# Optimization experiments

Measured on AMD Instinct MI355X. Metric: run time of the kernel, lower is better.

Reference implementation:

```python
import jax, jax.numpy as jnp
import numpy as np

D_MODEL = 2048
N_HEADS = 16
D_HEAD = 128
ROPE_THETA = 10000.0


def _rope(x, offset):
    # x: [B, H, S, D]; half-rotation RoPE with position offset
    B, H, S, D = x.shape
    inv_freq = 1.0 / (ROPE_THETA ** (jnp.arange(0, D, 2, dtype=jnp.float32) / D))  # [D/2]
    pos = (offset + jnp.arange(S, dtype=jnp.float32))                              # [S]
    ang = pos[:, None] * inv_freq[None, :]                                         # [S, D/2]
    cos = jnp.cos(ang).astype(x.dtype)
    sin = jnp.sin(ang).astype(x.dtype)
    x1, x2 = x[..., : D // 2], x[..., D // 2 :]
    return jnp.concatenate([x1 * cos - x2 * sin, x2 * cos + x1 * sin], axis=-1)


def setup_inputs() -> dict:
    key = jax.random.key(0)
    ks = jax.random.split(key, 5)
    B, Sq, Skv = 4, 1024, 1024
    x = jax.random.normal(ks[0], (B, Sq, D_MODEL), dtype=jnp.float32)
    cache_k = jax.random.normal(ks[1], (B, N_HEADS, Skv, D_HEAD), dtype=jnp.float32)
    cache_v = jax.random.normal(ks[2], (B, N_HEADS, Skv, D_HEAD), dtype=jnp.float32)
    w_qkv = jax.random.normal(ks[3], (D_MODEL, 3 * D_MODEL), dtype=jnp.float32) * (D_MODEL ** -0.5)
    w_o = jax.random.normal(ks[4], (D_MODEL, D_MODEL), dtype=jnp.float32) * (D_MODEL ** -0.5)
    return {"x": x, "cache_k": cache_k, "cache_v": cache_v, "w_qkv": w_qkv, "w_o": w_o}


def reference(x, cache_k, cache_v, w_qkv, w_o):
    B, S, _ = x.shape
    offset = cache_k.shape[2]
    # fused QKV projection: [B, S, 3*d_model] -> [B, H, S, 3*d_head]
    qkv = jnp.einsum("bsd,de->bse", x, w_qkv)
    qkv = qkv.reshape(B, S, N_HEADS, 3 * D_HEAD).transpose(0, 2, 1, 3)
    q, k, v = jnp.split(qkv, 3, axis=-1)
    q = _rope(q, offset)
    k = _rope(k, offset)
    # KV-cache concat along sequence dim
    k = jnp.concatenate([cache_k, k], axis=2)  # [B, H, Skv+S, D]
    v = jnp.concatenate([cache_v, v], axis=2)
    # SDPA (no mask, matching mask=None path)
    scale = D_HEAD ** -0.5
    scores = jnp.einsum("bhqd,bhkd->bhqk", q, k) * scale
    attn = jax.nn.softmax(scores, axis=-1)
    out = jnp.einsum("bhqk,bhkd->bhqd", attn, v)           # [B, H, S, D]
    out = out.transpose(0, 2, 1, 3).reshape(B, S, D_MODEL)
    return jnp.einsum("bsd,de->bse", out, w_o)
```

## Files before the change

kernel.cpp:

```cpp
#include <hip/hip_runtime.h>


typedef __bf16 bf16x8 __attribute__((ext_vector_type(8)));
typedef float f32x4 __attribute__((ext_vector_type(4)));
typedef unsigned short u16x8 __attribute__((ext_vector_type(8)));
typedef unsigned short u16x4 __attribute__((ext_vector_type(4)));

__device__ __forceinline__ float b2f(unsigned short u) {
  return __builtin_bit_cast(float, (unsigned int)u << 16);
}
__device__ __forceinline__ unsigned short f2b(float f) {
  unsigned int x = __builtin_bit_cast(unsigned int, f);
  x += 0x7fffu + ((x >> 16) & 1u);
  return (unsigned short)(x >> 16);
}
__device__ __forceinline__ unsigned int cvt_pk_bf16(float lo, float hi) {
  unsigned int r;
  asm("v_cvt_pk_bf16_f32 %0, %1, %2" : "=v"(r) : "v"(lo), "v"(hi));
  return r;
}
__device__ __forceinline__ void gload_lds16(const void* g, void* l) {
  __builtin_amdgcn_global_load_lds(
      (__attribute__((address_space(1))) void*)(g),
      (__attribute__((address_space(3))) void*)(l), 16, 0, 0);
}
__device__ __forceinline__ void barrier_nodrain() {
  asm volatile("" ::: "memory");
  __builtin_amdgcn_s_barrier();
  asm volatile("" ::: "memory");
}

__global__ void build_trig(float* __restrict__ cs, float* __restrict__ sn) {
  int idx = blockIdx.x * 256 + threadIdx.x;
  int s = idx >> 6, i = idx & 63;
  float inv = exp2f(-(float)i * (13.287712379549449f / 64.0f));
  float ang = (float)(1024 + s) * inv;
  cs[idx] = cosf(ang);
  sn[idx] = sinf(ang);
}

__global__ void conv_bf16(const float* __restrict__ in, unsigned short* __restrict__ out) {
  size_t i = ((size_t)blockIdx.x * 256 + threadIdx.x) * 8;
  float4 a = *(const float4*)(in + i);
  float4 b = *(const float4*)(in + i + 4);
  u16x8 v;
  v[0] = f2b(a.x); v[1] = f2b(a.y); v[2] = f2b(a.z); v[3] = f2b(a.w);
  v[4] = f2b(b.x); v[5] = f2b(b.y); v[6] = f2b(b.z); v[7] = f2b(b.w);
  *(u16x8*)(out + i) = v;
}

__global__ __launch_bounds__(256) void transpose_conv(
    const float* __restrict__ in, unsigned short* __restrict__ out, int R, int C) {
  __shared__ float tile[32][33];
  int c0 = blockIdx.x * 32, r0 = blockIdx.y * 32;
  int tx = threadIdx.x & 31, ty = threadIdx.x >> 5;
#pragma unroll
  for (int j = 0; j < 4; ++j)
    tile[ty + j * 8][tx] = in[(size_t)(r0 + ty + j * 8) * C + c0 + tx];
  __syncthreads();
#pragma unroll
  for (int j = 0; j < 4; ++j)
    out[(size_t)(c0 + ty + j * 8) * R + r0 + tx] = f2b(tile[tx][ty + j * 8]);
}

__global__ void copy_k(const float* __restrict__ ck, unsigned short* __restrict__ Kf) {
  size_t idx = ((size_t)blockIdx.x * 256 + threadIdx.x) * 4;
  size_t bh = idx >> 17, rem = idx & 131071;
  float4 a = *(const float4*)(ck + idx);
  u16x4 v;
  v[0] = f2b(a.x); v[1] = f2b(a.y); v[2] = f2b(a.z); v[3] = f2b(a.w);
  *(u16x4*)(Kf + bh * 262144 + rem) = v;
}

__global__ __launch_bounds__(256) void rope_qk(
    const unsigned short* __restrict__ qkv, const float* __restrict__ cs,
    const float* __restrict__ sn, unsigned short* __restrict__ Qb,
    unsigned short* __restrict__ Kf) {
  int row = blockIdx.x;
  int b = row >> 10, s = row & 1023;
#pragma unroll
  for (int it = 0; it < 4; ++it) {
    int item = it * 256 + threadIdx.x;
    int h = item >> 6, i = item & 63;
    const unsigned short* base = qkv + (size_t)row * 6144 + h * 384;
    float q1 = b2f(base[i]),       q2 = b2f(base[64 + i]);
    float k1 = b2f(base[128 + i]), k2 = b2f(base[192 + i]);
    float c = cs[s * 64 + i], sv = sn[s * 64 + i];
    const float scale = 0.12751738f;
    size_t bh = (size_t)(b * 16 + h);
    unsigned short* qd = Qb + (bh * 1024 + s) * 128;
    qd[i]      = f2b((q1 * c - q2 * sv) * scale);
    qd[64 + i] = f2b((q2 * c + q1 * sv) * scale);
    unsigned short* kd = Kf + (bh * 2048 + 1024 + s) * 128;
    kd[i]      = f2b(k1 * c - k2 * sv);
    kd[64 + i] = f2b(k2 * c + k1 * sv);
  }
}

__global__ __launch_bounds__(256) void build_vt(
    const float* __restrict__ cv, const unsigned short* __restrict__ qkv,
    unsigned short* __restrict__ Vt) {
  __shared__ float tile[32][33];
  int bhid = blockIdx.z;
  int s0 = blockIdx.x * 32, d0 = blockIdx.y * 32;
  int tx = threadIdx.x & 31, ty = threadIdx.x >> 5;
  int b = bhid >> 4, h = bhid & 15;
#pragma unroll
  for (int j = 0; j < 4; ++j) {
    int s = s0 + ty + j * 8, d = d0 + tx;
    float v;
    if (s < 1024) v = cv[((size_t)bhid * 1024 + s) * 128 + d];
    else v = b2f(qkv[((size_t)b * 1024 + (s - 1024)) * 6144 + h * 384 + 256 + d]);
    tile[ty + j * 8][tx] = v;
  }
  __syncthreads();
#pragma unroll
  for (int j = 0; j < 4; ++j) {
    int d = d0 + ty + j * 8, s = s0 + tx;
    Vt[((size_t)bhid * 128 + d) * 2048 + s] = f2b(tile[tx][ty + j * 8]);
  }
}

template <int M, int N, int K, bool OUT_BF16>
__global__ __launch_bounds__(512, 4) void gemm_ring(
    const unsigned short* __restrict__ A, const unsigned short* __restrict__ B,
    void* __restrict__ Cout) {
  __shared__ __align__(16) char lds[3 * 24576];
  constexpr int NT = N / 128;
  constexpr int Kt = K / 32;
  int bid = blockIdx.x;
  int tm = bid / NT, tn = bid % NT;
  int tid = threadIdx.x;
  int lane = tid & 63, wave = tid >> 6;
  int wr = (wave >> 1) * 64, wc = (wave & 1) * 64;
  int l15 = lane & 15, g = lane >> 4;

  int p = tid * 16;
  const unsigned short* aSrc0 = A + (size_t)(tm * 256 + (p >> 6)) * K + ((p & 63) >> 1);
  const unsigned short* aSrc1 = aSrc0 + (size_t)128 * K;
  const unsigned short* bSrc  = B + (size_t)(tn * 128 + (p >> 6)) * K + ((p & 63) >> 1);

  f32x4 acc[4][4] = {};

  auto stage = [&](int s) {
    char* base = (char*)lds + s * 24576;
    gload_lds16(aSrc0, base + p);
    gload_lds16(aSrc1, base + 8192 + p);
    gload_lds16(bSrc,  base + 16384 + p);
    aSrc0 += 32; aSrc1 += 32; bSrc += 32;
  };

  stage(0);
  stage(1);
  asm volatile("s_waitcnt vmcnt(3)" ::: "memory");

  int slot = 0, sNext = 2;
  for (int t = 0; t < Kt; ++t) {
    barrier_nodrain();
    if (t + 2 < Kt) {
      stage(sNext);
      sNext = (sNext == 2) ? 0 : sNext + 1;
      asm volatile("s_waitcnt vmcnt(3)" ::: "memory");
    } else {
      asm volatile("s_waitcnt vmcnt(0)" ::: "memory");
    }
    const char* As_ = (const char*)lds + slot * 24576;
    const char* Bs_ = As_ + 16384;
    bf16x8 af[4], bfr[4];
#pragma unroll
    for (int m = 0; m < 4; ++m)
      af[m] = *(const bf16x8*)(As_ + (wr + m * 16 + l15) * 64 + g * 16);
#pragma unroll
    for (int n = 0; n < 4; ++n)
      bfr[n] = *(const bf16x8*)(Bs_ + (wc + n * 16 + l15) * 64 + g * 16);
    __builtin_amdgcn_s_setprio(1);
#pragma unroll
    for (int m = 0; m < 4; ++m)
#pragma unroll
      for (int n = 0; n < 4; ++n)
        acc[m][n] = __builtin_amdgcn_mfma_f32_16x16x32_bf16(af[m], bfr[n], acc[m][n], 0, 0, 0);
    __builtin_amdgcn_s_setprio(0);
    slot = (slot == 2) ? 0 : slot + 1;
  }

#pragma unroll
  for (int m = 0; m < 4; ++m) {
    int row0 = tm * 256 + wr + m * 16 + g * 4;
#pragma unroll
    for (int n = 0; n < 4; ++n) {
      int col = tn * 128 + wc + n * 16 + l15;
#pragma unroll
      for (int r = 0; r < 4; ++r) {
        size_t off = (size_t)(row0 + r) * N + col;
        if constexpr (OUT_BF16) ((unsigned short*)Cout)[off] = f2b(acc[m][n][r]);
        else ((float*)Cout)[off] = acc[m][n][r];
      }
    }
  }
}

__global__ __launch_bounds__(256, 2) void attn_kernel(
    const unsigned short* __restrict__ Qb,
    const unsigned short* __restrict__ Kf,
    const unsigned short* __restrict__ Vt,
    unsigned short* __restrict__ Out) {
  __shared__ __align__(16) unsigned short Ks[2][64 * 128];
  __shared__ __align__(16) unsigned short Vs[2][64 * 128];
  __shared__ __align__(16) char PsRaw[4 * 2048];

  int bid = blockIdx.x;
  bid = (bid & 7) * 128 + (bid >> 3);
  int bh = bid >> 4, qt = bid & 15;
  int tid = threadIdx.x, lane = tid & 63, wave = tid >> 6;
  int l15 = lane & 15, g = lane >> 4;
  int swz = (l15 & 7) << 4;

  bf16x8 qf[4];
  const unsigned short* qp = Qb + ((size_t)(bh * 1024 + qt * 64 + wave * 16 + l15)) * 128;
#pragma unroll
  for (int kk = 0; kk < 4; ++kk)
    qf[kk] = *(const bf16x8*)(qp + kk * 32 + g * 8);

  u16x8 ou;
#pragma unroll
  for (int j = 0; j < 8; ++j) ou[j] = 0x3F80;
  bf16x8 ones = __builtin_bit_cast(bf16x8, ou);

  const unsigned short* Kbase = Kf + (size_t)bh * 2048 * 128;
  const unsigned short* Vbase = Vt + (size_t)bh * 128 * 2048;
  const unsigned short* kptr[4];
  const unsigned short* vptr[4];
  char* kdst0[4];
  char* vdst0[4];
#pragma unroll
  for (int is = 0; is < 4; ++is) {
    int p = tid * 16 + is * 4096;
    int lgk = p ^ (((p >> 8) & 7) << 4);
    kptr[is] = Kbase + (size_t)(lgk >> 8) * 128 + ((lgk & 255) >> 1);
    kdst0[is] = (char*)Ks + is * 4096 + (tid & 192) * 16;
    int lgv = p ^ (((p >> 7) & 7) << 4);
    vptr[is] = Vbase + (size_t)(lgv >> 7) * 2048 + ((lgv & 127) >> 1);
    vdst0[is] = (char*)Vs + is * 4096 + (tid & 192) * 16;
  }
  char* ps = PsRaw + wave * 2048 + l15 * 128;

  auto stage = [&](int buf) {
#pragma unroll
    for (int is = 0; is < 4; ++is) {
      gload_lds16(kptr[is], kdst0[is] + buf * 16384);  kptr[is] += 64 * 128;
      gload_lds16(vptr[is], vdst0[is] + buf * 16384);  vptr[is] += 64;
    }
  };

  float mrun = -1e30f;
  f32x4 acc[8] = {};
  f32x4 acc_l = {};

  stage(0);
  for (int it = 0; it < 32; ++it) {
    int cur = it & 1;
    barrier_nodrain();
    if (it + 1 < 32) {
      stage(cur ^ 1);
      asm volatile("s_waitcnt vmcnt(8)" ::: "memory");
    } else {
      asm volatile("s_waitcnt vmcnt(0)" ::: "memory");
    }
    barrier_nodrain();
    const char* ksA = (const char*)Ks + cur * 16384 + l15 * 256;
    const char* vsA = (const char*)Vs + cur * 16384 + l15 * 128;

    f32x4 st[4] = {};
#pragma unroll
    for (int kk = 0; kk < 4; ++kk) {
#pragma unroll
      for (int t = 0; t < 4; ++t) {
        bf16x8 a = *(const bf16x8*)(ksA + t * 4096 + ((kk * 64 + g * 16) ^ swz));
        st[t] = __builtin_amdgcn_mfma_f32_16x16x32_bf16(a, qf[kk], st[t], 0, 0, 0);
      }
    }

    float m0 = fmaxf(fmaxf(st[0][0], st[0][1]), st[0][2]);
    float m1 = fmaxf(fmaxf(st[0][3], st[1][0]), st[1][1]);
    float m2 = fmaxf(fmaxf(st[1][2], st[1][3]), st[2][0]);
    float m3 = fmaxf(fmaxf(st[2][1], st[2][2]), st[2][3]);
    float m4 = fmaxf(fmaxf(st[3][0], st[3][1]), st[3][2]);
    float pmax = fmaxf(fmaxf(fmaxf(m0, m1), fmaxf(m2, m3)), fmaxf(m4, st[3][3]));
    pmax = fmaxf(pmax, __shfl_xor(pmax, 16));
    pmax = fmaxf(pmax, __shfl_xor(pmax, 32));

    if (!__all(pmax - mrun <= 8.0f)) {
      float mnew = fmaxf(mrun, pmax);
      float corr = exp2f(mrun - mnew);
      acc_l *= corr;
#pragma unroll
      for (int mt = 0; mt < 8; ++mt) acc[mt] *= corr;
      mrun = mnew;
    }

    float pv[4][4];
#pragma unroll
    for (int t = 0; t < 4; ++t) {
      pv[t][0] = exp2f(st[t][0] - mrun);
      pv[t][1] = exp2f(st[t][1] - mrun);
      pv[t][2] = exp2f(st[t][2] - mrun);
      pv[t][3] = exp2f(st[t][3] - mrun);
    }

#pragma unroll
    for (int t = 0; t < 4; ++t) {
      uint2 w;
      w.x = cvt_pk_bf16(pv[t][0], pv[t][1]);
      w.y = cvt_pk_bf16(pv[t][2], pv[t][3]);
      *(uint2*)(ps + ((t * 32 + g * 8) ^ swz)) = w;
    }

#pragma unroll
    for (int k2 = 0; k2 < 2; ++k2) {
      bf16x8 pfr = *(const bf16x8*)(ps + ((k2 * 64 + g * 16) ^ swz));
      acc_l = __builtin_amdgcn_mfma_f32_16x16x32_bf16(ones, pfr, acc_l, 0, 0, 0);
#pragma unroll
      for (int mt = 0; mt < 8; ++mt) {
        bf16x8 a = *(const bf16x8*)(vsA + mt * 2048 + ((k2 * 64 + g * 16) ^ swz));
        acc[mt] = __builtin_amdgcn_mfma_f32_16x16x32_bf16(a, pfr, acc[mt], 0, 0, 0);
      }
    }
  }

  float inv = 1.f / acc_l[0];
  int b = bh >> 4, h = bh & 15;
  int sq = qt * 64 + wave * 16 + l15;
  unsigned short* orow = Out + ((size_t)(b * 1024 + sq) * 16 + h) * 128;
#pragma unroll
  for (int mt = 0; mt < 8; ++mt) {
    uint2 w;
    w.x = cvt_pk_bf16(acc[mt][0] * inv, acc[mt][1] * inv);
    w.y = cvt_pk_bf16(acc[mt][2] * inv, acc[mt][3] * inv);
    *(uint2*)(orow + mt * 16 + g * 4) = w;
  }
}

extern "C" void kernel_launch(void* const* d_in, const int* in_sizes, int n_in,
                              void* d_out, int out_size, void* d_ws, size_t ws_size,
                              hipStream_t stream) {
  const float* x       = (const float*)d_in[0];
  const float* cache_k = (const float*)d_in[1];
  const float* cache_v = (const float*)d_in[2];
  const float* w_qkv   = (const float*)d_in[3];
  const float* w_o     = (const float*)d_in[4];
  float* out = (float*)d_out;

  char* W = (char*)d_ws;
  constexpr size_t O_TRIG = 0;
  constexpr size_t O_XB   = 524288;
  constexpr size_t O_WQT  = O_XB  + 16777216;
  constexpr size_t O_WOT  = O_WQT + 25165824;
  constexpr size_t O_QKV  = O_WOT + 8388608;
  constexpr size_t O_QB   = O_QKV + 50331648;
  constexpr size_t O_KF   = O_QB  + 16777216;
  constexpr size_t O_VT   = O_KF  + 33554432;
  float* cs_tab = (float*)(W + O_TRIG);
  float* sn_tab = (float*)(W + O_TRIG + 262144);
  unsigned short* xb   = (unsigned short*)(W + O_XB);
  unsigned short* wqT  = (unsigned short*)(W + O_WQT);
  unsigned short* woT  = (unsigned short*)(W + O_WOT);
  unsigned short* qkv  = (unsigned short*)(W + O_QKV);
  unsigned short* qb   = (unsigned short*)(W + O_QB);
  unsigned short* Kf   = (unsigned short*)(W + O_KF);
  unsigned short* Vt   = (unsigned short*)(W + O_VT);
  unsigned short* attn_out = xb;

  build_trig<<<256, 256, 0, stream>>>(cs_tab, sn_tab);
  conv_bf16<<<4096, 256, 0, stream>>>(x, xb);
  transpose_conv<<<dim3(192, 64), 256, 0, stream>>>(w_qkv, wqT, 2048, 6144);
  transpose_conv<<<dim3(64, 64), 256, 0, stream>>>(w_o, woT, 2048, 2048);
  gemm_ring<4096, 6144, 2048, true><<<768, 512, 0, stream>>>(xb, wqT, qkv);
  rope_qk<<<4096, 256, 0, stream>>>(qkv, cs_tab, sn_tab, qb, Kf);
  copy_k<<<8192, 256, 0, stream>>>(cache_k, Kf);
  build_vt<<<dim3(64, 4, 64), 256, 0, stream>>>(cache_v, qkv, Vt);
  attn_kernel<<<1024, 256, 0, stream>>>(qb, Kf, Vt, attn_out);
  gemm_ring<4096, 2048, 2048, false><<<256, 512, 0, stream>>>(attn_out, woT, out);
}
```

Baseline: 359.3 us.

## Process two 16-row query tiles per wave in attention to reuse K/V loads

Each wave now handles 32 query rows (two 16-row MFMA tiles) instead of 16, so each block covers 128 query rows and the grid is halved to 512 blocks. Every K and V fragment read from LDS feeds two MFMAs, and each K/V tile staged from global memory is shared by twice as many queries, cutting LDS and global traffic per query. The cost is doubled accumulator registers, which may pressure occupancy under launch_bounds(256,2), more LDS for the P buffers, and fewer blocks across the CUs.

Result: faster. 335.7 us (-6.6%).

```diff
diff --git a/kernel.cpp b/kernel.cpp
--- a/kernel.cpp
+++ b/kernel.cpp
@@ -206,20 +206,23 @@
     unsigned short* __restrict__ Out) {
   __shared__ __align__(16) unsigned short Ks[2][64 * 128];
   __shared__ __align__(16) unsigned short Vs[2][64 * 128];
-  __shared__ __align__(16) char PsRaw[4 * 2048];
-
-  int bid = blockIdx.x;
-  bid = (bid & 7) * 128 + (bid >> 3);
-  int bh = bid >> 4, qt = bid & 15;
+  __shared__ __align__(16) char PsRaw[4 * 2 * 2048];
+
+  int raw = blockIdx.x;
+  int sb = (raw & 7) * 64 + (raw >> 3);
+  int bh = sb >> 3, qt = sb & 7;
   int tid = threadIdx.x, lane = tid & 63, wave = tid >> 6;
   int l15 = lane & 15, g = lane >> 4;
   int swz = (l15 & 7) << 4;
 
-  bf16x8 qf[4];
-  const unsigned short* qp = Qb + ((size_t)(bh * 1024 + qt * 64 + wave * 16 + l15)) * 128;
-#pragma unroll
-  for (int kk = 0; kk < 4; ++kk)
-    qf[kk] = *(const bf16x8*)(qp + kk * 32 + g * 8);
+  int qrow0 = qt * 128 + wave * 32;
+  bf16x8 qf0[4], qf1[4];
+  const unsigned short* qp0 = Qb + ((size_t)(bh * 1024 + qrow0 + l15)) * 128;
+#pragma unroll
+  for (int kk = 0; kk < 4; ++kk) {
+    qf0[kk] = *(const bf16x8*)(qp0 + kk * 32 + g * 8);
+    qf1[kk] = *(const bf16x8*)(qp0 + 16 * 128 + kk * 32 + g * 8);
+  }
 
   u16x8 ou;
 #pragma unroll
@@ -242,7 +245,8 @@
     vptr[is] = Vbase + (size_t)(lgv >> 7) * 2048 + ((lgv & 127) >> 1);
     vdst0[is] = (char*)Vs + is * 4096 + (tid & 192) * 16;
   }
-  char* ps = PsRaw + wave * 2048 + l15 * 128;
+  char* ps0 = PsRaw + wave * 4096 + l15 * 128;
+  char* ps1 = ps0 + 2048;
 
   auto stage = [&](int buf) {
 #pragma unroll
@@ -252,9 +256,40 @@
     }
   };
 
-  float mrun = -1e30f;
-  f32x4 acc[8] = {};
-  f32x4 acc_l = {};
+  float mrun0 = -1e30f, mrun1 = -1e30f;
+  f32x4 acc0[8] = {}, acc1[8] = {};
+  f32x4 accl0 = {}, accl1 = {};
+
+  auto softmax_pack = [&](f32x4* st, float& mrun, f32x4* accp, f32x4& accl,
+                          char* ps) {
+    float m0 = fmaxf(fmaxf(st[0][0], st[0][1]), st[0][2]);
+    float m1 = fmaxf(fmaxf(st[0][3], st[1][0]), st[1][1]);
+    float m2 = fmaxf(fmaxf(st[1][2], st[1][3]), st[2][0]);
+    float m3 = fmaxf(fmaxf(st[2][1], st[2][2]), st[2][3]);
+    float m4 = fmaxf(fmaxf(st[3][0], st[3][1]), st[3][2]);
+    float pmax = fmaxf(fmaxf(fmaxf(m0, m1), fmaxf(m2, m3)), fmaxf(m4, st[3][3]));
+    pmax = fmaxf(pmax, __shfl_xor(pmax, 16));
+    pmax = fmaxf(pmax, __shfl_xor(pmax, 32));
+    if (!__all(pmax - mrun <= 8.0f)) {
+      float mnew = fmaxf(mrun, pmax);
+      float corr = exp2f(mrun - mnew);
+      accl *= corr;
+#pragma unroll
+      for (int mt = 0; mt < 8; ++mt) accp[mt] *= corr;
+      mrun = mnew;
+    }
+#pragma unroll
+    for (int t = 0; t < 4; ++t) {
+      float p0 = exp2f(st[t][0] - mrun);
+      float p1 = exp2f(st[t][1] - mrun);
+      float p2 = exp2f(st[t][2] - mrun);
+      float p3 = exp2f(st[t][3] - mrun);
+      uint2 w;
+      w.x = cvt_pk_bf16(p0, p1);
+      w.y = cvt_pk_bf16(p2, p3);
+      *(uint2*)(ps + ((t * 32 + g * 8) ^ swz)) = w;
+    }
+  };
 
   stage(0);
   for (int it = 0; it < 32; ++it) {
@@ -270,73 +305,50 @@
     const char* ksA = (const char*)Ks + cur * 16384 + l15 * 256;
     const char* vsA = (const char*)Vs + cur * 16384 + l15 * 128;
 
-    f32x4 st[4] = {};
+    f32x4 st0[4] = {}, st1[4] = {};
 #pragma unroll
     for (int kk = 0; kk < 4; ++kk) {
 #pragma unroll
       for (int t = 0; t < 4; ++t) {
         bf16x8 a = *(const bf16x8*)(ksA + t * 4096 + ((kk * 64 + g * 16) ^ swz));
-        st[t] = __builtin_amdgcn_mfma_f32_16x16x32_bf16(a, qf[kk], st[t], 0, 0, 0);
+        st0[t] = __builtin_amdgcn_mfma_f32_16x16x32_bf16(a, qf0[kk], st0[t], 0, 0, 0);
+        st1[t] = __builtin_amdgcn_mfma_f32_16x16x32_bf16(a, qf1[kk], st1[t], 0, 0, 0);
       }
     }
 
-    float m0 = fmaxf(fmaxf(st[0][0], st[0][1]), st[0][2]);
-    float m1 = fmaxf(fmaxf(st[0][3], st[1][0]), st[1][1]);
-    float m2 = fmaxf(fmaxf(st[1][2], st[1][3]), st[2][0]);
-    float m3 = fmaxf(fmaxf(st[2][1], st[2][2]), st[2][3]);
-    float m4 = fmaxf(fmaxf(st[3][0], st[3][1]), st[3][2]);
-    float pmax = fmaxf(fmaxf(fmaxf(m0, m1), fmaxf(m2, m3)), fmaxf(m4, st[3][3]));
-    pmax = fmaxf(pmax, __shfl_xor(pmax, 16));
-    pmax = fmaxf(pmax, __shfl_xor(pmax, 32));
-
-    if (!__all(pmax - mrun <= 8.0f)) {
-      float mnew = fmaxf(mrun, pmax);
-      float corr = exp2f(mrun - mnew);
-      acc_l *= corr;
-#pragma unroll
-      for (int mt = 0; mt < 8; ++mt) acc[mt] *= corr;
-      mrun = mnew;
-    }
-
-    float pv[4][4];
-#pragma unroll
-    for (int t = 0; t < 4; ++t) {
-      pv[t][0] = exp2f(st[t][0] - mrun);
-      pv[t][1] = exp2f(st[t][1] - mrun);
-      pv[t][2] = exp2f(st[t][2] - mrun);
-      pv[t][3] = exp2f(st[t][3] - mrun);
-    }
-
-#pragma unroll
-    for (int t = 0; t < 4; ++t) {
-      uint2 w;
-      w.x = cvt_pk_bf16(pv[t][0], pv[t][1]);
-      w.y = cvt_pk_bf16(pv[t][2], pv[t][3]);
-      *(uint2*)(ps + ((t * 32 + g * 8) ^ swz)) = w;
-    }
+    softmax_pack(st0, mrun0, acc0, accl0, ps0);
+    softmax_pack(st1, mrun1, acc1, accl1, ps1);
 
 #pragma unroll
     for (int k2 = 0; k2 < 2; ++k2) {
-      bf16x8 pfr = *(const bf16x8*)(ps + ((k2 * 64 + g * 16) ^ swz));
-      acc_l = __builtin_amdgcn_mfma_f32_16x16x32_bf16(ones, pfr, acc_l, 0, 0, 0);
+      bf16x8 p0 = *(const bf16x8*)(ps0 + ((k2 * 64 + g * 16) ^ swz));
+      bf16x8 p1 = *(const bf16x8*)(ps1 + ((k2 * 64 + g * 16) ^ swz));
+      accl0 = __builtin_amdgcn_mfma_f32_16x16x32_bf16(ones, p0, accl0, 0, 0, 0);
+      accl1 = __builtin_amdgcn_mfma_f32_16x16x32_bf16(ones, p1, accl1, 0, 0, 0);
 #pragma unroll
       for (int mt = 0; mt < 8; ++mt) {
         bf16x8 a = *(const bf16x8*)(vsA + mt * 2048 + ((k2 * 64 + g * 16) ^ swz));
-        acc[mt] = __builtin_amdgcn_mfma_f32_16x16x32_bf16(a, pfr, acc[mt], 0, 0, 0);
+        acc0[mt] = __builtin_amdgcn_mfma_f32_16x16x32_bf16(a, p0, acc0[mt], 0, 0, 0);
+        acc1[mt] = __builtin_amdgcn_mfma_f32_16x16x32_bf16(a, p1, acc1[mt], 0, 0, 0);
       }
     }
   }
 
-  float inv = 1.f / acc_l[0];
+  float inv0 = 1.f / accl0[0];
+  float inv1 = 1.f / accl1[0];
   int b = bh >> 4, h = bh & 15;
-  int sq = qt * 64 + wave * 16 + l15;
-  unsigned short* orow = Out + ((size_t)(b * 1024 + sq) * 16 + h) * 128;
+  int sq = qt * 128 + wave * 32 + l15;
+  unsigned short* orow0 = Out + ((size_t)(b * 1024 + sq) * 16 + h) * 128;
+  unsigned short* orow1 = orow0 + (size_t)16 * 2048;
 #pragma unroll
   for (int mt = 0; mt < 8; ++mt) {
-    uint2 w;
-    w.x = cvt_pk_bf16(acc[mt][0] * inv, acc[mt][1] * inv);
-    w.y = cvt_pk_bf16(acc[mt][2] * inv, acc[mt][3] * inv);
-    *(uint2*)(orow + mt * 16 + g * 4) = w;
+    uint2 w0, w1;
+    w0.x = cvt_pk_bf16(acc0[mt][0] * inv0, acc0[mt][1] * inv0);
+    w0.y = cvt_pk_bf16(acc0[mt][2] * inv0, acc0[mt][3] * inv0);
+    w1.x = cvt_pk_bf16(acc1[mt][0] * inv1, acc1[mt][1] * inv1);
+    w1.y = cvt_pk_bf16(acc1[mt][2] * inv1, acc1[mt][3] * inv1);
+    *(uint2*)(orow0 + mt * 16 + g * 4) = w0;
+    *(uint2*)(orow1 + mt * 16 + g * 4) = w1;
   }
 }
 
@@ -378,6 +390,6 @@
   rope_qk<<<4096, 256, 0, stream>>>(qkv, cs_tab, sn_tab, qb, Kf);
   copy_k<<<8192, 256, 0, stream>>>(cache_k, Kf);
   build_vt<<<dim3(64, 4, 64), 256, 0, stream>>>(cache_v, qkv, Vt);
-  attn_kernel<<<1024, 256, 0, stream>>>(qb, Kf, Vt, attn_out);
+  attn_kernel<<<512, 256, 0, stream>>>(qb, Kf, Vt, attn_out);
   gemm_ring<4096, 2048, 2048, false><<<256, 512, 0, stream>>>(attn_out, woT, out);
 }
```
